# Kernel tuning notes

Measured on AMD Instinct MI355X. Metric: run time of the kernel, lower is better.

## Reference

```python
import jax, jax.numpy as jnp
import numpy as np

NUM_HEADS = 12
NUM_PATCHES = 196


def _make_relative_distance_index(num_patches=NUM_PATCHES):
    size = int(np.sqrt(num_patches))  # 14
    coords = np.stack(np.meshgrid(np.arange(size), np.arange(size), indexing='ij'))  # [2,14,14]
    flat = coords.reshape(2, -1)  # [2,196]
    rel = flat[:, None, :] - flat[:, :, None]  # [2,196,196]
    rel = rel.transpose(1, 2, 0).astype(np.int64)  # [196,196,2]
    rel[:, :, 0] += size - 1
    rel[:, :, 1] += size - 1
    rel[:, :, 0] *= 2 * size - 1
    idx = rel.sum(-1) + 1  # shift for cls slot at table row 0
    full = np.zeros((num_patches + 1, num_patches + 1), dtype=np.int64)
    full[1:, 1:] = idx
    return full


def setup_inputs() -> dict:
    key = jax.random.key(0)
    k1, k2, k3, k4, k5 = jax.random.split(key, 5)
    B, N, C = 64, NUM_PATCHES + 1, 768
    table_size = (2 * int(np.sqrt(NUM_PATCHES)) - 1) ** 2 + 1  # 730
    x = jax.random.normal(k1, (B, N, C), dtype=jnp.float32)
    table = jax.random.normal(k2, (table_size, NUM_HEADS), dtype=jnp.float32) * 0.02
    w_qkv = jax.random.normal(k3, (3 * C, C), dtype=jnp.float32) * 0.02
    w_proj = jax.random.normal(k4, (C, C), dtype=jnp.float32) * 0.02
    b_proj = jax.random.normal(k5, (C,), dtype=jnp.float32) * 0.02
    rel_index = jnp.asarray(_make_relative_distance_index())
    return {"x": x, "table": table, "w_qkv": w_qkv, "w_proj": w_proj,
            "b_proj": b_proj, "rel_index": rel_index}


def reference(x, table, w_qkv, w_proj, b_proj, rel_index):
    B, N, C = x.shape
    H = NUM_HEADS
    hd = C // H
    scale = hd ** -0.5
    # qkv projection: [B,N,3C] -> [3,B,H,N,hd]
    qkv = (x @ w_qkv.T).reshape(B, N, 3, H, hd).transpose(2, 0, 3, 1, 4)
    q, k, v = qkv[0], qkv[1], qkv[2]
    # gathered relative position bias: [N,N,H] -> [H,N,N]
    bias = table[rel_index].transpose(2, 0, 1)
    scores = jnp.einsum('bhnd,bhmd->bhnm', q, k) * scale + bias[None]
    attn = jax.nn.softmax(scores, axis=-1)
    out = jnp.einsum('bhnm,bhmd->bhnd', attn, v)
    out = out.transpose(0, 2, 1, 3).reshape(B, N, C)
    return out @ w_proj.T + b_proj
```

## Files before the change

### kernel.cpp

```cpp
#include <hip/hip_runtime.h>


#define NB   64
#define NN   197
#define NC   768
#define NH   12
#define HD   64
#define MM   (NB*NN)
#define MR   12672
#define NP   208
#define WV   208
#define SZQ  ((size_t)NB * NH * NN * HD)

typedef unsigned short ushort_t;
typedef __attribute__((ext_vector_type(8))) short short8;
typedef __attribute__((ext_vector_type(4))) float f32x4;
union U128 { uint4 u; short8 s; };

__device__ __forceinline__ unsigned bf16_rne(float f) {
    unsigned u = __float_as_uint(f);
    return (u + 0x7fffu + ((u >> 16) & 1u)) >> 16;
}

__device__ __forceinline__ void gld16(unsigned short* lds, const unsigned short* g) {
    __builtin_amdgcn_global_load_lds(
        (const __attribute__((address_space(1))) void*)g,
        (__attribute__((address_space(3))) void*)lds, 16, 0, 0);
}

__global__ __launch_bounds__(256) void convert_all(
    const float* __restrict__ x, const float* __restrict__ w_qkv,
    const float* __restrict__ w_proj,
    ushort_t* __restrict__ xh, ushort_t* __restrict__ wh,
    ushort_t* __restrict__ wp)
{
    int idx = blockIdx.x * 256 + threadIdx.x;
    if (idx >= (MM + 2304 + 768) * 192) return;
    int r = idx / 192;
    int c = (idx - r * 192) * 4;
    const float* src;
    ushort_t* dsth;
    if (r < MM) {
        src = x + (size_t)r * NC; dsth = xh + (size_t)r * NC + c;
    } else if (r < MM + 2304) {
        int rr = r - MM;
        src = w_qkv + (size_t)rr * NC; dsth = wh + (size_t)rr * NC + c;
    } else {
        int rr = r - MM - 2304;
        src = w_proj + (size_t)rr * NC; dsth = wp + (size_t)rr * NC + c;
    }
    float4 f = *(const float4*)(src + c);
    ushort4 hv = { (ushort_t)bf16_rne(f.x), (ushort_t)bf16_rne(f.y),
                   (ushort_t)bf16_rne(f.z), (ushort_t)bf16_rne(f.w) };
    *(ushort4*)dsth = hv;
}

__global__ __launch_bounds__(256) void bias_precompute(
    const float* __restrict__ table, const int* __restrict__ rel_index,
    float* __restrict__ biasP)
{
    int i = blockIdx.x * 256 + threadIdx.x;
    if (i >= NH * 13 * 13 * 256) return;
    int r = i & 3, l15 = (i >> 2) & 15, quad = (i >> 6) & 3;
    int t = i >> 8;
    int kt = t % 13; int t2 = t / 13;
    int qt = t2 % 13; int h = t2 / 13;
    int n = qt * 16 + quad * 4 + r;
    int m = kt * 16 + l15;
    float v = -1e30f;
    if (n < NN && m < NN) v = table[rel_index[n * NN + m] * NH + h];
    biasP[i] = v;
}

__device__ __forceinline__ void gemm_mainloop(
    const ushort_t* __restrict__ A2, int sA,
    const ushort_t* __restrict__ B2, int sB,
    int m0, int n0, int kiters, ushort_t* Abuf, ushort_t* Bbuf, f32x4 acc[4][4])
{
    const int tid = threadIdx.x;
    const int w = tid >> 6, lane = tid & 63;
    const int wm = w & 1, wn = w >> 1;
    const int lr = lane >> 3, lc = lane & 7;
    const int gch = lc ^ lr;

    const ushort_t* Ag = A2 + (size_t)(m0 + w * 32 + lr) * sA + gch * 8;
    const ushort_t* Bg = B2 + (size_t)(n0 + w * 32 + lr) * sB + gch * 8;
    ushort_t* Al = Abuf + (w * 32) * 64;
    ushort_t* Bl = Bbuf + (w * 32) * 64;

    int aoff[4], boff[4];
    const int quad = lane >> 4, l15 = lane & 15;
    #pragma unroll
    for (int t = 0; t < 4; t++) {
        int ra = wm * 64 + t * 16 + l15;
        aoff[t] = ra * 64 + ((quad ^ (ra & 7)) << 3);
        int rb = wn * 64 + t * 16 + l15;
        boff[t] = rb * 64 + ((quad ^ (rb & 7)) << 3);
    }

    for (int ks = 0; ks < kiters; ks++) {
        __syncthreads();
        #pragma unroll
        for (int it = 0; it < 4; it++) {
            gld16(Al + it * 8 * 64, Ag + (size_t)it * 8 * sA);
            gld16(Bl + it * 8 * 64, Bg + (size_t)it * 8 * sB);
        }
        __syncthreads();
        #pragma unroll
        for (int k0 = 0; k0 < 2; k0++) {
            U128 af[4], bf[4];
            #pragma unroll
            for (int t = 0; t < 4; t++) {
                af[t].u = *(const uint4*)&Abuf[aoff[t] ^ (k0 << 5)];
                bf[t].u = *(const uint4*)&Bbuf[boff[t] ^ (k0 << 5)];
            }
            #pragma unroll
            for (int i = 0; i < 4; i++)
                #pragma unroll
                for (int j = 0; j < 4; j++)
                    acc[i][j] = __builtin_amdgcn_mfma_f32_16x16x32_bf16(
                        af[i].s, bf[j].s, acc[i][j], 0, 0, 0);
        }
        Ag += 64; Bg += 64;
    }
}

__global__ __launch_bounds__(256) void gemm_qkv_mfma(
    const ushort_t* __restrict__ A2, const ushort_t* __restrict__ B2,
    ushort_t* __restrict__ qbf, ushort_t* __restrict__ kbf,
    ushort_t* __restrict__ vbf)
{
    __shared__ ushort_t Abuf[128 * 64];
    __shared__ ushort_t Bbuf[128 * 64];
    f32x4 acc[4][4];
    f32x4 z = {0.f, 0.f, 0.f, 0.f};
    #pragma unroll
    for (int i = 0; i < 4; i++)
        #pragma unroll
        for (int j = 0; j < 4; j++) acc[i][j] = z;

    const int m0 = blockIdx.y * 128, n0 = blockIdx.x * 128;
    gemm_mainloop(A2, NC, B2, NC, m0, n0, 12, Abuf, Bbuf, acc);

    const int tid = threadIdx.x;
    const int w = tid >> 6, lane = tid & 63;
    const int wm = w & 1, wn = w >> 1;
    const int quad = lane >> 4, l15 = lane & 15;

    size_t baseo[4][4];
    bool valid[4][4];
    #pragma unroll
    for (int mt = 0; mt < 4; mt++) {
        #pragma unroll
        for (int r = 0; r < 4; r++) {
            int m = m0 + wm * 64 + mt * 16 + quad * 4 + r;
            valid[mt][r] = (m < MM);
            int mc = valid[mt][r] ? m : 0;
            int b_ = mc / NN, n_ = mc - b_ * NN;
            baseo[mt][r] = ((size_t)b_ * NH * NN + n_) * HD;
        }
    }
    #pragma unroll
    for (int nt = 0; nt < 4; nt++) {
        int c0 = n0 + wn * 64 + nt * 16;
        int tq = c0 / NC;
        int wi = c0 - tq * NC;
        int hh = wi >> 6;
        int d0 = (wi & 63) + l15;
        ushort_t* dst = (tq == 0) ? qbf : (tq == 1) ? kbf : vbf;
        float scale = (tq == 0) ? 0.125f : 1.0f;
        size_t hoff = (size_t)hh * (NN * HD) + d0;
        #pragma unroll
        for (int mt = 0; mt < 4; mt++) {
            #pragma unroll
            for (int r = 0; r < 4; r++) {
                if (valid[mt][r])
                    dst[baseo[mt][r] + hoff] = (ushort_t)bf16_rne(acc[mt][nt][r] * scale);
            }
        }
    }
}

__global__ __launch_bounds__(256) void gemm_proj_mfma(
    const ushort_t* __restrict__ A2, const ushort_t* __restrict__ B2,
    const float* __restrict__ bias, float* __restrict__ out)
{
    __shared__ ushort_t Abuf[128 * 64];
    __shared__ ushort_t Bbuf[128 * 64];
    f32x4 acc[4][4];
    f32x4 z = {0.f, 0.f, 0.f, 0.f};
    #pragma unroll
    for (int i = 0; i < 4; i++)
        #pragma unroll
        for (int j = 0; j < 4; j++) acc[i][j] = z;

    const int m0 = blockIdx.y * 128, n0 = blockIdx.x * 128;
    gemm_mainloop(A2, NC, B2, NC, m0, n0, 12, Abuf, Bbuf, acc);

    const int tid = threadIdx.x;
    const int w = tid >> 6, lane = tid & 63;
    const int wm = w & 1, wn = w >> 1;
    const int quad = lane >> 4, l15 = lane & 15;
    #pragma unroll
    for (int nt = 0; nt < 4; nt++) {
        int col = n0 + wn * 64 + nt * 16 + l15;
        float bi = bias[col];
        #pragma unroll
        for (int mt = 0; mt < 4; mt++) {
            #pragma unroll
            for (int r = 0; r < 4; r++) {
                int m = m0 + wm * 64 + mt * 16 + quad * 4 + r;
                if (m < MM)
                    out[(size_t)m * NC + col] = acc[mt][nt][r] + bi;
            }
        }
    }
}

__global__ __launch_bounds__(256) void attn_mfma(
    const ushort_t* __restrict__ qbf, const ushort_t* __restrict__ kbf,
    const ushort_t* __restrict__ vbf, const float* __restrict__ biasP,
    ushort_t* __restrict__ ab)
{
    __shared__ ushort_t Vt[64 * WV];
    __shared__ ushort_t Pl[4][16 * WV];

    const int bh = blockIdx.x;
    const int b = bh / NH, h = bh % NH;
    const int tid = threadIdx.x;
    const int w = tid >> 6, lane = tid & 63;
    const int quad = lane >> 4, l15 = lane & 15;
    const size_t base = (size_t)bh * (NN * HD);
    const ushort_t* kg = kbf + base;
    const ushort_t* vg = vbf + base;
    const ushort_t* qg = qbf + base;

    ushort_t* Vstage = &Pl[0][0];
    for (int idx = tid; idx < NP * 8; idx += 256) {
        int row = idx >> 3, ch = idx & 7;
        uint4 val = {0u, 0u, 0u, 0u};
        if (row < NN) val = *(const uint4*)(vg + (size_t)row * HD + ch * 8);
        *(uint4*)&Vstage[row * HD + ch * 8] = val;
    }
    __syncthreads();
    for (int task = tid; task < 64 * 26; task += 256) {
        int d = task & 63, kc = task >> 6;
        ushort_t tmp[8];
        #pragma unroll
        for (int j = 0; j < 8; j++)
            tmp[j] = Vstage[(kc * 8 + j) * HD + d];
        uint4 u;
        u.x = (unsigned)tmp[0] | ((unsigned)tmp[1] << 16);
        u.y = (unsigned)tmp[2] | ((unsigned)tmp[3] << 16);
        u.z = (unsigned)tmp[4] | ((unsigned)tmp[5] << 16);
        u.w = (unsigned)tmp[6] | ((unsigned)tmp[7] << 16);
        *(uint4*)&Vt[d * WV + kc * 8] = u;
    }
    __syncthreads();

    #pragma unroll
    for (int rep = 0; rep < 4; rep++) {
        int qt = w + rep * 4;
        if (qt > 12) break;
        const int q0 = qt * 16;

        int qrow = q0 + l15; if (qrow > NN - 1) qrow = NN - 1;
        U128 qf0, qf1;
        qf0.u = *(const uint4*)(qg + (size_t)qrow * HD + quad * 8);
        qf1.u = *(const uint4*)(qg + (size_t)qrow * HD + 32 + quad * 8);

        f32x4 S[13];
        const float* bp = biasP + ((size_t)(h * 13 + qt) * 13) * 256 + (quad << 6) + (l15 << 2);
        #pragma unroll
        for (int kt = 0; kt < 13; kt++) {
            float4 bv = *(const float4*)(bp + kt * 256);
            S[kt][0] = bv.x; S[kt][1] = bv.y; S[kt][2] = bv.z; S[kt][3] = bv.w;
        }

        #pragma unroll
        for (int kt = 0; kt < 13; kt++) {
            int krow = kt * 16 + l15; if (krow > NN - 1) krow = NN - 1;
            U128 k0, k1;
            k0.u = *(const uint4*)(kg + (size_t)krow * HD + quad * 8);
            k1.u = *(const uint4*)(kg + (size_t)krow * HD + 32 + quad * 8);
            S[kt] = __builtin_amdgcn_mfma_f32_16x16x32_bf16(qf0.s, k0.s, S[kt], 0, 0, 0);
            S[kt] = __builtin_amdgcn_mfma_f32_16x16x32_bf16(qf1.s, k1.s, S[kt], 0, 0, 0);
        }

        ushort_t* P = Pl[w];
        #pragma unroll
        for (int r = 0; r < 4; r++) {
            float mx = S[0][r];
            #pragma unroll
            for (int kt = 1; kt < 13; kt++) mx = fmaxf(mx, S[kt][r]);
            mx = fmaxf(mx, __shfl_xor(mx, 1));
            mx = fmaxf(mx, __shfl_xor(mx, 2));
            mx = fmaxf(mx, __shfl_xor(mx, 4));
            mx = fmaxf(mx, __shfl_xor(mx, 8));
            float sum = 0.f;
            #pragma unroll
            for (int kt = 0; kt < 13; kt++) {
                float e = __expf(S[kt][r] - mx);
                S[kt][r] = e;
                sum += e;
            }
            sum += __shfl_xor(sum, 1);
            sum += __shfl_xor(sum, 2);
            sum += __shfl_xor(sum, 4);
            sum += __shfl_xor(sum, 8);
            float inv = 1.0f / sum;
            int prow = quad * 4 + r;
            #pragma unroll
            for (int kt = 0; kt < 13; kt++)
                P[prow * WV + kt * 16 + l15] = (ushort_t)bf16_rne(S[kt][r] * inv);
        }

        f32x4 O[4];
        f32x4 z4 = {0.f, 0.f, 0.f, 0.f};
        #pragma unroll
        for (int dt = 0; dt < 4; dt++) O[dt] = z4;
        #pragma unroll
        for (int ks = 0; ks < 7; ks++) {
            int pc = ks * 32 + quad * 8;
            bool vld = (pc < NP);
            int pcc = vld ? pc : 0;
            U128 pf;
            pf.u = *(const uint4*)&P[l15 * WV + pcc];
            if (!vld) { pf.u.x = 0u; pf.u.y = 0u; pf.u.z = 0u; pf.u.w = 0u; }
            #pragma unroll
            for (int dt = 0; dt < 4; dt++) {
                U128 vf;
                vf.u = *(const uint4*)&Vt[(dt * 16 + l15) * WV + pcc];
                O[dt] = __builtin_amdgcn_mfma_f32_16x16x32_bf16(pf.s, vf.s, O[dt], 0, 0, 0);
            }
        }

        float* Osh = (float*)&Pl[w][0];
        #pragma unroll
        for (int dt = 0; dt < 4; dt++)
            #pragma unroll
            for (int r = 0; r < 4; r++)
                Osh[(quad * 4 + r) * 68 + dt * 16 + l15] = O[dt][r];
        int orow = lane >> 2;
        int d0 = (lane & 3) << 4;
        int q = q0 + orow;
        if (q < NN) {
            unsigned hiw[8];
            #pragma unroll
            for (int k4 = 0; k4 < 4; k4++) {
                float4 f = *(const float4*)&Osh[orow * 68 + d0 + k4 * 4];
                unsigned h0 = bf16_rne(f.x), h1 = bf16_rne(f.y);
                unsigned h2 = bf16_rne(f.z), h3 = bf16_rne(f.w);
                hiw[k4 * 2]     = h0 | (h1 << 16);
                hiw[k4 * 2 + 1] = h2 | (h3 << 16);
            }
            size_t baseo = ((size_t)b * NN + q) * NC + h * HD + d0;
            uint4 hA = {hiw[0], hiw[1], hiw[2], hiw[3]};
            uint4 hB = {hiw[4], hiw[5], hiw[6], hiw[7]};
            *(uint4*)&ab[baseo] = hA;
            *(uint4*)&ab[baseo + 8] = hB;
        }
    }
}

extern "C" void kernel_launch(void* const* d_in, const int* in_sizes, int n_in,
                              void* d_out, int out_size, void* d_ws, size_t ws_size,
                              hipStream_t stream)
{
    const float* x        = (const float*)d_in[0];
    const float* table    = (const float*)d_in[1];
    const float* w_qkv    = (const float*)d_in[2];
    const float* w_proj   = (const float*)d_in[3];
    const float* b_proj   = (const float*)d_in[4];
    const int*   rel_idx  = (const int*)d_in[5];
    float* out = (float*)d_out;

    ushort_t* xh  = (ushort_t*)d_ws;
    ushort_t* wh  = xh + (size_t)MR * NC;
    ushort_t* wp  = wh + (size_t)2304 * NC;
    ushort_t* ab  = wp + (size_t)768 * NC;
    ushort_t* qbf = ab + (size_t)MR * NC;
    ushort_t* kbf = qbf + SZQ;
    ushort_t* vbf = kbf + SZQ;
    float* biasP  = (float*)(vbf + SZQ);

    const int cvt_quads = (MM + 2304 + 768) * 192;
    convert_all<<<(cvt_quads + 255) / 256, 256, 0, stream>>>(
        x, w_qkv, w_proj, xh, wh, wp);
    bias_precompute<<<(NH * 13 * 13 * 256 + 255) / 256, 256, 0, stream>>>(
        table, rel_idx, biasP);

    gemm_qkv_mfma<<<dim3(18, 99), 256, 0, stream>>>(xh, wh, qbf, kbf, vbf);
    attn_mfma<<<768, 256, 0, stream>>>(qbf, kbf, vbf, biasP, ab);
    gemm_proj_mfma<<<dim3(6, 99), 256, 0, stream>>>(ab, wp, b_proj, out);
}
```

Baseline: 280.2 us.

## Merge prep kernels, remap GEMM blocks per XCD, stage QKV stores through LDS

Merges the bf16 conversion and bias-precompute kernels into a single launch. Both GEMMs now use a 1D grid with an XCD-aware block remap so neighbouring tiles share an L2. The QKV epilogue writes tiles into LDS and then emits 16-byte coalesced row stores in place of scattered 2-byte stores. The attention kernel pads the Vt stride to cut LDS bank conflicts, batches its K loads ahead of the MFMAs, and adds an occupancy hint. The cost is an extra __syncthreads and LDS reuse in the epilogue, plus higher register pressure from holding 13 K fragments at once.

```diff
diff --git a/kernel.cpp b/kernel.cpp
--- a/kernel.cpp
+++ b/kernel.cpp
@@ -9,8 +9,11 @@
 #define MM   (NB*NN)
 #define MR   12672
 #define NP   208
-#define WV   208
+#define PS   208
+#define VTS  216
 #define SZQ  ((size_t)NB * NH * NN * HD)
+#define CVTQ ((MM + 2304 + 768) * 192)
+#define BIASN (NH * 13 * 13 * 256)
 
 typedef unsigned short ushort_t;
 typedef __attribute__((ext_vector_type(8))) short short8;
@@ -28,48 +31,46 @@
         (__attribute__((address_space(3))) void*)lds, 16, 0, 0);
 }
 
-__global__ __launch_bounds__(256) void convert_all(
+__global__ __launch_bounds__(256) void prepare(
     const float* __restrict__ x, const float* __restrict__ w_qkv,
-    const float* __restrict__ w_proj,
+    const float* __restrict__ w_proj, const float* __restrict__ table,
+    const int* __restrict__ rel_index,
     ushort_t* __restrict__ xh, ushort_t* __restrict__ wh,
-    ushort_t* __restrict__ wp)
+    ushort_t* __restrict__ wp, float* __restrict__ biasP)
 {
     int idx = blockIdx.x * 256 + threadIdx.x;
-    if (idx >= (MM + 2304 + 768) * 192) return;
-    int r = idx / 192;
-    int c = (idx - r * 192) * 4;
-    const float* src;
-    ushort_t* dsth;
-    if (r < MM) {
-        src = x + (size_t)r * NC; dsth = xh + (size_t)r * NC + c;
-    } else if (r < MM + 2304) {
-        int rr = r - MM;
-        src = w_qkv + (size_t)rr * NC; dsth = wh + (size_t)rr * NC + c;
+    if (idx < CVTQ) {
+        int r = idx / 192;
+        int c = (idx - r * 192) * 4;
+        const float* src;
+        ushort_t* dsth;
+        if (r < MM) {
+            src = x + (size_t)r * NC; dsth = xh + (size_t)r * NC + c;
+        } else if (r < MM + 2304) {
+            int rr = r - MM;
+            src = w_qkv + (size_t)rr * NC; dsth = wh + (size_t)rr * NC + c;
+        } else {
+            int rr = r - MM - 2304;
+            src = w_proj + (size_t)rr * NC; dsth = wp + (size_t)rr * NC + c;
+        }
+        float4 f = *(const float4*)(src + c);
+        ushort4 hv = { (ushort_t)bf16_rne(f.x), (ushort_t)bf16_rne(f.y),
+                       (ushort_t)bf16_rne(f.z), (ushort_t)bf16_rne(f.w) };
+        *(ushort4*)dsth = hv;
     } else {
-        int rr = r - MM - 2304;
-        src = w_proj + (size_t)rr * NC; dsth = wp + (size_t)rr * NC + c;
-    }
-    float4 f = *(const float4*)(src + c);
-    ushort4 hv = { (ushort_t)bf16_rne(f.x), (ushort_t)bf16_rne(f.y),
-                   (ushort_t)bf16_rne(f.z), (ushort_t)bf16_rne(f.w) };
-    *(ushort4*)dsth = hv;
-}
-
-__global__ __launch_bounds__(256) void bias_precompute(
-    const float* __restrict__ table, const int* __restrict__ rel_index,
-    float* __restrict__ biasP)
-{
-    int i = blockIdx.x * 256 + threadIdx.x;
-    if (i >= NH * 13 * 13 * 256) return;
-    int r = i & 3, l15 = (i >> 2) & 15, quad = (i >> 6) & 3;
-    int t = i >> 8;
-    int kt = t % 13; int t2 = t / 13;
-    int qt = t2 % 13; int h = t2 / 13;
-    int n = qt * 16 + quad * 4 + r;
-    int m = kt * 16 + l15;
-    float v = -1e30f;
-    if (n < NN && m < NN) v = table[rel_index[n * NN + m] * NH + h];
-    biasP[i] = v;
+        int i = idx - CVTQ;
+        if (i < BIASN) {
+            int r = i & 3, l15 = (i >> 2) & 15, quad = (i >> 6) & 3;
+            int t = i >> 8;
+            int kt = t % 13; int t2 = t / 13;
+            int qt = t2 % 13; int h = t2 / 13;
+            int n = qt * 16 + quad * 4 + r;
+            int m = kt * 16 + l15;
+            float v = -1e30f;
+            if (n < NN && m < NN) v = table[rel_index[n * NN + m] * NH + h];
+            biasP[i] = v;
+        }
+    }
 }
 
 __device__ __forceinline__ void gemm_mainloop(
@@ -125,6 +126,12 @@
     }
 }
 
+__device__ __forceinline__ int xcd_remap(int bid, int nwg) {
+    int q8 = nwg >> 3, r8 = nwg & 7;
+    int xcd = bid & 7, loc = bid >> 3;
+    return (xcd < r8 ? xcd * (q8 + 1) : r8 * (q8 + 1) + (xcd - r8) * q8) + loc;
+}
+
 __global__ __launch_bounds__(256) void gemm_qkv_mfma(
     const ushort_t* __restrict__ A2, const ushort_t* __restrict__ B2,
     ushort_t* __restrict__ qbf, ushort_t* __restrict__ kbf,
@@ -139,44 +146,44 @@
         #pragma unroll
         for (int j = 0; j < 4; j++) acc[i][j] = z;
 
-    const int m0 = blockIdx.y * 128, n0 = blockIdx.x * 128;
+    int f = xcd_remap(blockIdx.x, 1782);
+    int mt_ = f / 18, nt_ = f - mt_ * 18;
+    const int m0 = mt_ * 128, n0 = nt_ * 128;
     gemm_mainloop(A2, NC, B2, NC, m0, n0, 12, Abuf, Bbuf, acc);
+
+    __syncthreads();
 
     const int tid = threadIdx.x;
     const int w = tid >> 6, lane = tid & 63;
     const int wm = w & 1, wn = w >> 1;
     const int quad = lane >> 4, l15 = lane & 15;
 
-    size_t baseo[4][4];
-    bool valid[4][4];
+    int c0b = n0 + wn * 64;
+    int tq = c0b / NC;
+    int wi = c0b - tq * NC;
+    int hh = wi >> 6;
+    ushort_t* dst = (tq == 0) ? qbf : (tq == 1) ? kbf : vbf;
+    float scale = (tq == 0) ? 0.125f : 1.0f;
+
+    ushort_t* Sw = Abuf + w * 1152;
+    const int orow = lane >> 2;
+    const int dch = (lane & 3) << 3;
     #pragma unroll
     for (int mt = 0; mt < 4; mt++) {
         #pragma unroll
-        for (int r = 0; r < 4; r++) {
-            int m = m0 + wm * 64 + mt * 16 + quad * 4 + r;
-            valid[mt][r] = (m < MM);
-            int mc = valid[mt][r] ? m : 0;
-            int b_ = mc / NN, n_ = mc - b_ * NN;
-            baseo[mt][r] = ((size_t)b_ * NH * NN + n_) * HD;
-        }
-    }
-    #pragma unroll
-    for (int nt = 0; nt < 4; nt++) {
-        int c0 = n0 + wn * 64 + nt * 16;
-        int tq = c0 / NC;
-        int wi = c0 - tq * NC;
-        int hh = wi >> 6;
-        int d0 = (wi & 63) + l15;
-        ushort_t* dst = (tq == 0) ? qbf : (tq == 1) ? kbf : vbf;
-        float scale = (tq == 0) ? 0.125f : 1.0f;
-        size_t hoff = (size_t)hh * (NN * HD) + d0;
-        #pragma unroll
-        for (int mt = 0; mt < 4; mt++) {
-            #pragma unroll
-            for (int r = 0; r < 4; r++) {
-                if (valid[mt][r])
-                    dst[baseo[mt][r] + hoff] = (ushort_t)bf16_rne(acc[mt][nt][r] * scale);
-            }
+        for (int nt = 0; nt < 4; nt++)
+            #pragma unroll
+            for (int r = 0; r < 4; r++)
+                Sw[(quad * 4 + r) * 72 + nt * 16 + l15] =
+                    (ushort_t)bf16_rne(acc[mt][nt][r] * scale);
+        int m = m0 + wm * 64 + mt * 16 + orow;
+        if (m < MM) {
+            int b_ = m / NN, n_ = m - b_ * NN;
+            size_t rb = ((size_t)(b_ * NH + hh) * NN + n_) * HD;
+            uint4 v0 = *(const uint4*)&Sw[orow * 72 + dch];
+            uint4 v1 = *(const uint4*)&Sw[orow * 72 + dch + 32];
+            *(uint4*)&dst[rb + dch] = v0;
+            *(uint4*)&dst[rb + dch + 32] = v1;
         }
     }
 }
@@ -194,7 +201,9 @@
         #pragma unroll
         for (int j = 0; j < 4; j++) acc[i][j] = z;
 
-    const int m0 = blockIdx.y * 128, n0 = blockIdx.x * 128;
+    int f = xcd_remap(blockIdx.x, 594);
+    int mt_ = f / 6, nt_ = f - mt_ * 6;
+    const int m0 = mt_ * 128, n0 = nt_ * 128;
     gemm_mainloop(A2, NC, B2, NC, m0, n0, 12, Abuf, Bbuf, acc);
 
     const int tid = threadIdx.x;
@@ -217,13 +226,13 @@
     }
 }
 
-__global__ __launch_bounds__(256) void attn_mfma(
+__global__ __launch_bounds__(256, 3) void attn_mfma(
     const ushort_t* __restrict__ qbf, const ushort_t* __restrict__ kbf,
     const ushort_t* __restrict__ vbf, const float* __restrict__ biasP,
     ushort_t* __restrict__ ab)
 {
-    __shared__ ushort_t Vt[64 * WV];
-    __shared__ ushort_t Pl[4][16 * WV];
+    __shared__ ushort_t Vt[64 * VTS];
+    __shared__ ushort_t Pl[4][16 * PS];
 
     const int bh = blockIdx.x;
     const int b = bh / NH, h = bh % NH;
@@ -254,7 +263,7 @@
         u.y = (unsigned)tmp[2] | ((unsigned)tmp[3] << 16);
         u.z = (unsigned)tmp[4] | ((unsigned)tmp[5] << 16);
         u.w = (unsigned)tmp[6] | ((unsigned)tmp[7] << 16);
-        *(uint4*)&Vt[d * WV + kc * 8] = u;
+        *(uint4*)&Vt[d * VTS + kc * 8] = u;
     }
     __syncthreads();
 
@@ -277,14 +286,24 @@
             S[kt][0] = bv.x; S[kt][1] = bv.y; S[kt][2] = bv.z; S[kt][3] = bv.w;
         }
 
-        #pragma unroll
-        for (int kt = 0; kt < 13; kt++) {
-            int krow = kt * 16 + l15; if (krow > NN - 1) krow = NN - 1;
-            U128 k0, k1;
-            k0.u = *(const uint4*)(kg + (size_t)krow * HD + quad * 8);
-            k1.u = *(const uint4*)(kg + (size_t)krow * HD + 32 + quad * 8);
-            S[kt] = __builtin_amdgcn_mfma_f32_16x16x32_bf16(qf0.s, k0.s, S[kt], 0, 0, 0);
-            S[kt] = __builtin_amdgcn_mfma_f32_16x16x32_bf16(qf1.s, k1.s, S[kt], 0, 0, 0);
+        {
+            U128 kf[13];
+            #pragma unroll
+            for (int kt = 0; kt < 13; kt++) {
+                int krow = kt * 16 + l15; if (krow > NN - 1) krow = NN - 1;
+                kf[kt].u = *(const uint4*)(kg + (size_t)krow * HD + quad * 8);
+            }
+            #pragma unroll
+            for (int kt = 0; kt < 13; kt++)
+                S[kt] = __builtin_amdgcn_mfma_f32_16x16x32_bf16(qf0.s, kf[kt].s, S[kt], 0, 0, 0);
+            #pragma unroll
+            for (int kt = 0; kt < 13; kt++) {
+                int krow = kt * 16 + l15; if (krow > NN - 1) krow = NN - 1;
+                kf[kt].u = *(const uint4*)(kg + (size_t)krow * HD + 32 + quad * 8);
+            }
+            #pragma unroll
+            for (int kt = 0; kt < 13; kt++)
+                S[kt] = __builtin_amdgcn_mfma_f32_16x16x32_bf16(qf1.s, kf[kt].s, S[kt], 0, 0, 0);
         }
 
         ushort_t* P = Pl[w];
@@ -312,7 +331,7 @@
             int prow = quad * 4 + r;
             #pragma unroll
             for (int kt = 0; kt < 13; kt++)
-                P[prow * WV + kt * 16 + l15] = (ushort_t)bf16_rne(S[kt][r] * inv);
+                P[prow * PS + kt * 16 + l15] = (ushort_t)bf16_rne(S[kt][r] * inv);
         }
 
         f32x4 O[4];
@@ -325,12 +344,12 @@
             bool vld = (pc < NP);
             int pcc = vld ? pc : 0;
             U128 pf;
-            pf.u = *(const uint4*)&P[l15 * WV + pcc];
+            pf.u = *(const uint4*)&P[l15 * PS + pcc];
             if (!vld) { pf.u.x = 0u; pf.u.y = 0u; pf.u.z = 0u; pf.u.w = 0u; }
             #pragma unroll
             for (int dt = 0; dt < 4; dt++) {
                 U128 vf;
-                vf.u = *(const uint4*)&Vt[(dt * 16 + l15) * WV + pcc];
+                vf.u = *(const uint4*)&Vt[(dt * 16 + l15) * VTS + pcc];
                 O[dt] = __builtin_amdgcn_mfma_f32_16x16x32_bf16(pf.s, vf.s, O[dt], 0, 0, 0);
             }
         }
@@ -384,13 +403,11 @@
     ushort_t* vbf = kbf + SZQ;
     float* biasP  = (float*)(vbf + SZQ);
 
-    const int cvt_quads = (MM + 2304 + 768) * 192;
-    convert_all<<<(cvt_quads + 255) / 256, 256, 0, stream>>>(
-        x, w_qkv, w_proj, xh, wh, wp);
-    bias_precompute<<<(NH * 13 * 13 * 256 + 255) / 256, 256, 0, stream>>>(
-        table, rel_idx, biasP);
-
-    gemm_qkv_mfma<<<dim3(18, 99), 256, 0, stream>>>(xh, wh, qbf, kbf, vbf);
+    const int ptot = CVTQ + BIASN;
+    prepare<<<(ptot + 255) / 256, 256, 0, stream>>>(
+        x, w_qkv, w_proj, table, rel_idx, xh, wh, wp, biasP);
+
+    gemm_qkv_mfma<<<1782, 256, 0, stream>>>(xh, wh, qbf, kbf, vbf);
     attn_mfma<<<768, 256, 0, stream>>>(qbf, kbf, vbf, biasP, ab);
-    gemm_proj_mfma<<<dim3(6, 99), 256, 0, stream>>>(ab, wp, b_proj, out);
-}
+    gemm_proj_mfma<<<594, 256, 0, stream>>>(ab, wp, b_proj, out);
+}
```

Measured after the change: 279.9 us. Within noise of the previous version (-0.1%).
